# Kernel tuning notes

Hardware: AMD Instinct MI355X
Metric: run time of the kernel (lower is better)

Reference implementation:

```python
import jax, jax.numpy as jnp
import numpy as np

HEADS = 16
D_MODEL = 1024
D_HEAD = D_MODEL // HEADS


def setup_inputs() -> dict:
    key = jax.random.key(0)
    ks = jax.random.split(key, 9)
    s_h = 1.0 / np.sqrt(D_HEAD)
    s_m = 1.0 / np.sqrt(D_MODEL)
    return {
        "x": jax.random.normal(ks[0], (4, 2048, D_MODEL), dtype=jnp.float32),
        "Wq": jax.random.uniform(ks[1], (D_HEAD, D_HEAD), jnp.float32, -s_h, s_h),
        "bq": jax.random.uniform(ks[2], (D_HEAD,), jnp.float32, -s_h, s_h),
        "Wk": jax.random.uniform(ks[3], (D_HEAD, D_HEAD), jnp.float32, -s_h, s_h),
        "bk": jax.random.uniform(ks[4], (D_HEAD,), jnp.float32, -s_h, s_h),
        "Wv": jax.random.uniform(ks[5], (D_HEAD, D_HEAD), jnp.float32, -s_h, s_h),
        "bv": jax.random.uniform(ks[6], (D_HEAD,), jnp.float32, -s_h, s_h),
        "Wp": jax.random.uniform(ks[7], (D_MODEL, D_MODEL), jnp.float32, -s_m, s_m),
        "bp": jax.random.uniform(ks[8], (D_MODEL,), jnp.float32, -s_m, s_m),
    }


def reference(x, Wq, bq, Wk, bk, Wv, bv, Wp, bp):
    B, T, C = x.shape
    xh = x.reshape(B, T, HEADS, D_HEAD)  # [B,T,H,Dh]
    # per-head linear projections (torch Linear: x @ W.T + b)
    q = jnp.einsum('bthd,ed->bhte', xh, Wq) + bq  # [B,H,T,Dh]
    k = jnp.einsum('bthd,ed->bhte', xh, Wk) + bk
    v = jnp.einsum('bthd,ed->bhte', xh, Wv) + bv
    # NOTE: original scales by sqrt(C) = sqrt(d_model), not sqrt(d_head)
    att = jnp.einsum('bhqd,bhkd->bhqk', q, k) / jnp.sqrt(jnp.float32(C))
    att = jax.nn.softmax(att, axis=-1)
    out = jnp.einsum('bhqk,bhkd->bhqd', att, v)  # [B,H,T,Dh]
    out = out.transpose(0, 2, 1, 3).reshape(B, T, C)
    return out @ Wp.T + bp
```

## Files before the change

### kernel.cpp

```cpp
#include <hip/hip_runtime.h>
#include <hip/hip_bf16.h>
#include <cstddef>

#define B_  4
#define T_  2048
#define H_  16
#define DH  64
#define C_  1024
#define BH  64

typedef float  f32x16 __attribute__((ext_vector_type(16)));
typedef __bf16 bf16x8 __attribute__((ext_vector_type(8)));
typedef __bf16 bf16x4 __attribute__((ext_vector_type(4)));

#define MFMA32(a, b, c) __builtin_amdgcn_mfma_f32_32x32x16_bf16(a, b, c, 0, 0, 0)


__device__ __forceinline__ unsigned cvt_pk_bf16(float lo, float hi) {
    unsigned r;
    asm("v_cvt_pk_bf16_f32 %0, %1, %2" : "=v"(r) : "v"(lo), "v"(hi));
    return r;
}

__global__ __launch_bounds__(256) void wconv_kernel(
    const float* __restrict__ Wq, const float* __restrict__ Wk,
    const float* __restrict__ Wv, __bf16* __restrict__ wqkv)
{
    const int tid = blockIdx.x * 256 + threadIdx.x;
    const float* srcs[3] = {Wq, Wk, Wv};
    const int mat = tid >> 10;
    const int off = (tid & 1023) * 4;
    const float4 w4 = *(const float4*)(srcs[mat] + off);
    const unsigned lo = ((unsigned)__builtin_bit_cast(unsigned short, (__bf16)w4.y) << 16)
                      | (unsigned)__builtin_bit_cast(unsigned short, (__bf16)w4.x);
    const unsigned hi = ((unsigned)__builtin_bit_cast(unsigned short, (__bf16)w4.w) << 16)
                      | (unsigned)__builtin_bit_cast(unsigned short, (__bf16)w4.z);
    uint2 p; p.x = lo; p.y = hi;
    *(uint2*)(wqkv + mat * 4096 + off) = p;
}

__global__ __launch_bounds__(256) void qkv_kernel(
    const float* __restrict__ x,
    const __bf16* __restrict__ wqkv,
    const float* __restrict__ bq, const float* __restrict__ bk,
    const float* __restrict__ bv,
    __bf16* __restrict__ q, __bf16* __restrict__ kf, __bf16* __restrict__ vf)
{
    __shared__ __bf16 Xs[128 * 72];
    __shared__ __bf16 Ws[3][64 * 72];
    __bf16* Vtl = Xs;
    __bf16* Kst = &Ws[0][0];

    const int tt  = blockIdx.x;
    const int bh  = blockIdx.y;
    const int b   = bh >> 4, h = bh & 15;
    const int t0  = tt * 128;
    const int tid = threadIdx.x;
    const int wave = tid >> 6, lane = tid & 63;
    const int m = lane & 31, hh = lane >> 5;

    #pragma unroll
    for (int i = 0; i < 8; ++i) {
        const int idx = i * 256 + tid;
        const int r = idx >> 4, c = (idx & 15) * 4;
        const float4 x4 = *(const float4*)(x + ((size_t)(b * T_ + t0 + r)) * C_ + h * DH + c);
        const unsigned lo = ((unsigned)__builtin_bit_cast(unsigned short, (__bf16)x4.y) << 16)
                          | (unsigned)__builtin_bit_cast(unsigned short, (__bf16)x4.x);
        const unsigned hi = ((unsigned)__builtin_bit_cast(unsigned short, (__bf16)x4.w) << 16)
                          | (unsigned)__builtin_bit_cast(unsigned short, (__bf16)x4.z);
        *(unsigned*)&Xs[r * 72 + c]     = lo;
        *(unsigned*)&Xs[r * 72 + c + 2] = hi;
    }
    #pragma unroll
    for (int i = 0; i < 6; ++i) {
        const int idx = i * 256 + tid;
        const int mat_ = idx >> 9;
        const int r = (idx >> 3) & 63, c = (idx & 7) * 8;
        *(uint4*)&Ws[mat_][r * 72 + c] = *(const uint4*)(wqkv + mat_ * 4096 + r * 64 + c);
    }
    __syncthreads();

    bf16x8 xf[4];
    #pragma unroll
    for (int ks = 0; ks < 4; ++ks)
        xf[ks] = *(const bf16x8*)&Xs[(wave * 32 + m) * 72 + ks * 16 + hh * 8];
    __syncthreads();

    const float s32 = 0.03125f * 1.4426950408889634f;

    unsigned kpk[16];

    #pragma unroll
    for (int mat = 0; mat < 3; ++mat) {
        f32x16 acc0 = {}, acc1 = {};
        #pragma unroll
        for (int ks = 0; ks < 4; ++ks) {
            const bf16x8 w0 = *(const bf16x8*)&Ws[mat][(m) * 72 + ks * 16 + hh * 8];
            const bf16x8 w1 = *(const bf16x8*)&Ws[mat][(32 + m) * 72 + ks * 16 + hh * 8];
            acc0 = MFMA32(xf[ks], w0, acc0);
            acc1 = MFMA32(xf[ks], w1, acc1);
        }
        const float* bias = (mat == 0) ? bq : (mat == 1) ? bk : bv;
        const float b0 = bias[m], b1 = bias[32 + m];
        #pragma unroll
        for (int r = 0; r < 16; ++r) {
            const int R = (r & 3) + 8 * (r >> 2) + 4 * hh;
            const int tloc = wave * 32 + R;
            const float v0 = acc0[r] + b0, v1 = acc1[r] + b1;
            if (mat == 0) {
                const size_t base = ((size_t)bh * T_ + t0 + tloc) * DH;
                q[base + m]      = (__bf16)(v0 * s32);
                q[base + 32 + m] = (__bf16)(v1 * s32);
            } else if (mat == 1) {
                kpk[r] = ((unsigned)__builtin_bit_cast(unsigned short, (__bf16)v1) << 16)
                       |  (unsigned)__builtin_bit_cast(unsigned short, (__bf16)v0);
            } else {
                Vtl[(m) * 136 + tloc]      = (__bf16)v0;
                Vtl[(32 + m) * 136 + tloc] = (__bf16)v1;
            }
        }
    }
    __syncthreads();

    #pragma unroll
    for (int r = 0; r < 16; ++r) {
        const int R = (r & 3) + 8 * (r >> 2) + 4 * hh;
        const int tloc = wave * 32 + R;
        Kst[tloc * 72 + m]      = __builtin_bit_cast(__bf16, (unsigned short)(kpk[r] & 0xffff));
        Kst[tloc * 72 + 32 + m] = __builtin_bit_cast(__bf16, (unsigned short)(kpk[r] >> 16));
    }

    #pragma unroll
    for (int i = 0; i < 4; ++i) {
        const int idx = i * 256 + tid;
        const int ln = idx & 63, c_ = idx >> 6;
        const int kt64l = c_ >> 3, dh = (c_ >> 2) & 1, cN = c_ & 3;
        const __bf16* src = &Vtl[(dh * 32 + (ln & 31)) * 136 + kt64l * 64 + cN * 16 + (ln >> 5) * 8];
        __bf16* dst = vf + ((((size_t)(bh * 32 + tt * 2 + kt64l) * 2 + dh) * 4 + cN) * 64 + ln) * 8;
        *(uint4*)dst = *(const uint4*)src;
    }
    __syncthreads();

    #pragma unroll
    for (int i = 0; i < 4; ++i) {
        const int idx = i * 256 + tid;
        const int ln = idx & 63, c_ = idx >> 6;
        const int kt64l = c_ >> 3, rh = (c_ >> 2) & 1, ks = c_ & 3;
        const __bf16* src = &Kst[(kt64l * 64 + rh * 32 + (ln & 31)) * 72 + ks * 16 + (ln >> 5) * 8];
        __bf16* dst = kf + ((((size_t)(bh * 32 + tt * 2 + kt64l) * 2 + rh) * 4 + ks) * 64 + ln) * 8;
        *(uint4*)dst = *(const uint4*)src;
    }
}

__global__ __launch_bounds__(256, 4) void attn_kernel(
    const __bf16* __restrict__ q, const __bf16* __restrict__ kf,
    const __bf16* __restrict__ vf, __bf16* __restrict__ af)
{
    __shared__ float OL[2][64 * 36];
    __shared__ float LL[2][64];

    const int bh  = blockIdx.x;
    const int q0  = blockIdx.y * 64;
    const int tid = threadIdx.x;
    const int wave = tid >> 6, lane = tid & 63;
    const int m = lane & 31, h = lane >> 5;
    const int qs  = wave & 1;
    const int kvh = wave >> 1;

    const __bf16* qb  = q  + (size_t)bh * T_ * DH;
    const __bf16* kfb = kf + (size_t)bh * (T_ * DH);
    const __bf16* vfb = vf + (size_t)bh * (T_ * DH);

    bf16x8 qf[4];
    #pragma unroll
    for (int ks = 0; ks < 4; ++ks)
        qf[ks] = *(const bf16x8*)(qb + (size_t)(q0 + qs * 32 + m) * DH + ks * 16 + h * 8);

    f32x16 O0 = {}, O1 = {};
    float lsum = 0.f;

    const int ktEnd = kvh * 16 + 16;
    for (int kt = kvh * 16; kt < ktEnd; ++kt) {
        const __bf16* kt_k = kfb + kt * 4096;
        const __bf16* kt_v = vfb + kt * 4096;
        #pragma unroll
        for (int rh = 0; rh < 2; ++rh) {
            bf16x8 kfr[4];
            #pragma unroll
            for (int ks = 0; ks < 4; ++ks)
                kfr[ks] = *(const bf16x8*)(kt_k + rh * 2048 + ks * 512 + lane * 8);
            f32x16 S = {};
            #pragma unroll
            for (int ks = 0; ks < 4; ++ks)
                S = MFMA32(kfr[ks], qf[ks], S);

            #pragma unroll
            for (int cc = 0; cc < 2; ++cc) {
                const int rb = cc * 8;
                float e0 = __builtin_amdgcn_exp2f(S[rb + 0]);
                float e1 = __builtin_amdgcn_exp2f(S[rb + 1]);
                float e2 = __builtin_amdgcn_exp2f(S[rb + 2]);
                float e3 = __builtin_amdgcn_exp2f(S[rb + 3]);
                float e4 = __builtin_amdgcn_exp2f(S[rb + 4]);
                float e5 = __builtin_amdgcn_exp2f(S[rb + 5]);
                float e6 = __builtin_amdgcn_exp2f(S[rb + 6]);
                float e7 = __builtin_amdgcn_exp2f(S[rb + 7]);
                lsum += ((e0 + e1) + (e2 + e3)) + ((e4 + e5) + (e6 + e7));
                unsigned a0 = cvt_pk_bf16(e0, e1);
                unsigned a1 = cvt_pk_bf16(e2, e3);
                unsigned b0 = cvt_pk_bf16(e4, e5);
                unsigned b1 = cvt_pk_bf16(e6, e7);
                asm("v_permlane32_swap_b32 %0, %1" : "+v"(a0), "+v"(b0));
                asm("v_permlane32_swap_b32 %0, %1" : "+v"(a1), "+v"(b1));
                const uint4 pw = {a0, a1, b0, b1};
                const bf16x8 pb = __builtin_bit_cast(bf16x8, pw);
                const int c = rh * 2 + cc;
                const bf16x8 v0 = *(const bf16x8*)(kt_v + c * 512 + lane * 8);
                const bf16x8 v1 = *(const bf16x8*)(kt_v + 2048 + c * 512 + lane * 8);
                O0 = MFMA32(v0, pb, O0);
                O1 = MFMA32(v1, pb, O1);
            }
        }
    }

    if (kvh == 1) {
        #pragma unroll
        for (int g = 0; g < 4; ++g) {
            float4 p0, p1;
            p0.x = O0[4 * g];     p0.y = O0[4 * g + 1];
            p0.z = O0[4 * g + 2]; p0.w = O0[4 * g + 3];
            p1.x = O1[4 * g];     p1.y = O1[4 * g + 1];
            p1.z = O1[4 * g + 2]; p1.w = O1[4 * g + 3];
            *(float4*)&OL[qs][lane * 36 + 4 * g]      = p0;
            *(float4*)&OL[qs][lane * 36 + 16 + 4 * g] = p1;
        }
        LL[qs][lane] = lsum;
    }
    __syncthreads();
    if (kvh == 0) {
        #pragma unroll
        for (int g = 0; g < 4; ++g) {
            const float4 p0 = *(const float4*)&OL[qs][lane * 36 + 4 * g];
            const float4 p1 = *(const float4*)&OL[qs][lane * 36 + 16 + 4 * g];
            O0[4 * g]     += p0.x; O0[4 * g + 1] += p0.y;
            O0[4 * g + 2] += p0.z; O0[4 * g + 3] += p0.w;
            O1[4 * g]     += p1.x; O1[4 * g + 1] += p1.y;
            O1[4 * g + 2] += p1.z; O1[4 * g + 3] += p1.w;
        }
        lsum += LL[qs][lane];
        lsum += __shfl_xor(lsum, 32);
        const float linv = 1.0f / lsum;

        __bf16* ab = af + ((size_t)(bh * 16 + (q0 >> 7))) * 8192
                        + (((q0 >> 6) & 1) * 2 + qs) * 2048 + lane * 8;
        #pragma unroll
        for (int ks = 0; ks < 4; ++ks) {
            const f32x16& Og = (ks < 2) ? O0 : O1;
            const int rb = (ks & 1) * 8;
            unsigned a0 = cvt_pk_bf16(Og[rb + 0] * linv, Og[rb + 1] * linv);
            unsigned a1 = cvt_pk_bf16(Og[rb + 2] * linv, Og[rb + 3] * linv);
            unsigned b0 = cvt_pk_bf16(Og[rb + 4] * linv, Og[rb + 5] * linv);
            unsigned b1 = cvt_pk_bf16(Og[rb + 6] * linv, Og[rb + 7] * linv);
            asm("v_permlane32_swap_b32 %0, %1" : "+v"(a0), "+v"(b0));
            asm("v_permlane32_swap_b32 %0, %1" : "+v"(a1), "+v"(b1));
            const uint4 pw = {a0, a1, b0, b1};
            *(uint4*)(ab + ks * 512) = pw;
        }
    }
}

__global__ __launch_bounds__(256) void wpconv_kernel(
    const float* __restrict__ Wp, __bf16* __restrict__ wpf)
{
    const int ci = blockIdx.x * 256 + threadIdx.x;
    const int ln = ci & 63;
    const int ks = (ci >> 6) & 3;
    const int n  = (ci >> 8) & 3;
    const int cb = (ci >> 10) & 15;
    const int eb = ci >> 14;
    const int row = eb * 128 + n * 32 + (ln & 31);
    const int col = cb * 64 + ks * 16 + (ln >> 5) * 8;
    const float4 w0 = *(const float4*)(Wp + (size_t)row * C_ + col);
    const float4 w1 = *(const float4*)(Wp + (size_t)row * C_ + col + 4);
    uint4 p;
    p.x = ((unsigned)__builtin_bit_cast(unsigned short, (__bf16)w0.y) << 16)
        |  (unsigned)__builtin_bit_cast(unsigned short, (__bf16)w0.x);
    p.y = ((unsigned)__builtin_bit_cast(unsigned short, (__bf16)w0.w) << 16)
        |  (unsigned)__builtin_bit_cast(unsigned short, (__bf16)w0.z);
    p.z = ((unsigned)__builtin_bit_cast(unsigned short, (__bf16)w1.y) << 16)
        |  (unsigned)__builtin_bit_cast(unsigned short, (__bf16)w1.x);
    p.w = ((unsigned)__builtin_bit_cast(unsigned short, (__bf16)w1.w) << 16)
        |  (unsigned)__builtin_bit_cast(unsigned short, (__bf16)w1.z);
    *(uint4*)(wpf + (size_t)ci * 8) = p;
}

__global__ __launch_bounds__(256) void proj_kernel(
    const __bf16* __restrict__ af,
    const __bf16* __restrict__ wpf,
    const float* __restrict__ bp,
    float* __restrict__ out)
{
    const int tb2 = blockIdx.x, eb = blockIdx.y;
    const int tid = threadIdx.x;
    const int wave = tid >> 6, lane = tid & 63;
    const int m = lane & 31, h = lane >> 5;
    const int b = tb2 >> 5, rem = tb2 & 31;
    const int qtile = rem >> 1, half = rem & 1;
    const int wv = half * 2 + (wave & 1);
    const int eh = wave >> 1;
    const int e0 = eb * 128;

    const __bf16* abase = af + ((size_t)(b * 256 + qtile)) * 8192
                             + wv * 2048 + lane * 8;
    const __bf16* wbase = wpf + (size_t)eb * 131072 + eh * 4096 + lane * 8;

    f32x16 acc[2] = {f32x16{}, f32x16{}};

    for (int cb = 0; cb < 16; ++cb) {
        const __bf16* ap = abase + (size_t)cb * 131072;
        const __bf16* wp = wbase + (size_t)cb * 8192;
        bf16x8 afr[4];
        #pragma unroll
        for (int ks = 0; ks < 4; ++ks)
            afr[ks] = *(const bf16x8*)(ap + ks * 512);
        #pragma unroll
        for (int n = 0; n < 2; ++n) {
            #pragma unroll
            for (int ks = 0; ks < 4; ++ks) {
                const bf16x8 bf = *(const bf16x8*)(wp + (n * 4 + ks) * 512);
                acc[n] = MFMA32(afr[ks], bf, acc[n]);
            }
        }
    }

    const int tokbase = b * T_ + qtile * 128 + wv * 32;
    #pragma unroll
    for (int n = 0; n < 2; ++n) {
        const int e = e0 + (eh * 2 + n) * 32 + m;
        const float bias = bp[e];
        #pragma unroll
        for (int r = 0; r < 16; ++r) {
            const int R = (r & 3) + 8 * (r >> 2) + 4 * h;
            out[(size_t)(tokbase + R) * C_ + e] = acc[n][r] + bias;
        }
    }
}

extern "C" void kernel_launch(void* const* d_in, const int* in_sizes, int n_in,
                              void* d_out, int out_size, void* d_ws, size_t ws_size,
                              hipStream_t stream)
{
    const float* x  = (const float*)d_in[0];
    const float* Wq = (const float*)d_in[1];
    const float* bq = (const float*)d_in[2];
    const float* Wk = (const float*)d_in[3];
    const float* bk = (const float*)d_in[4];
    const float* Wv = (const float*)d_in[5];
    const float* bv = (const float*)d_in[6];
    const float* Wp = (const float*)d_in[7];
    const float* bp = (const float*)d_in[8];

    const size_t N = (size_t)BH * T_ * DH;
    __bf16* qws  = (__bf16*)d_ws;
    __bf16* kws  = qws + N;
    __bf16* vtws = kws + N;
    __bf16* aws  = vtws + N;
    __bf16* wqkv = aws;
    __bf16* wpf  = qws;

    wconv_kernel<<<dim3(12), 256, 0, stream>>>(Wq, Wk, Wv, wqkv);
    qkv_kernel<<<dim3(16, 64), 256, 0, stream>>>(
        x, wqkv, bq, bk, bv, qws, kws, vtws);
    attn_kernel<<<dim3(64, 32), 256, 0, stream>>>(qws, kws, vtws, aws);
    wpconv_kernel<<<dim3(512), 256, 0, stream>>>(Wp, wpf);
    proj_kernel<<<dim3(128, 8), 256, 0, stream>>>(aws, wpf, bp, (float*)d_out);
}
```

Measured before the change: 230.1 us.

## Give each attention wave 64 query rows over full KV; stage Wp conversion via LDS

After: 230.8 us. About the same (+0.3%).

```diff
diff --git a/kernel.cpp b/kernel.cpp
--- a/kernel.cpp
+++ b/kernel.cpp
@@ -152,35 +152,32 @@
     }
 }
 
-__global__ __launch_bounds__(256, 4) void attn_kernel(
+__global__ __launch_bounds__(256, 2) void attn_kernel(
     const __bf16* __restrict__ q, const __bf16* __restrict__ kf,
     const __bf16* __restrict__ vf, __bf16* __restrict__ af)
 {
-    __shared__ float OL[2][64 * 36];
-    __shared__ float LL[2][64];
-
     const int bh  = blockIdx.x;
-    const int q0  = blockIdx.y * 64;
+    const int q0  = blockIdx.y * 256;
     const int tid = threadIdx.x;
     const int wave = tid >> 6, lane = tid & 63;
     const int m = lane & 31, h = lane >> 5;
-    const int qs  = wave & 1;
-    const int kvh = wave >> 1;
+    const int row0 = q0 + wave * 64;
 
     const __bf16* qb  = q  + (size_t)bh * T_ * DH;
     const __bf16* kfb = kf + (size_t)bh * (T_ * DH);
     const __bf16* vfb = vf + (size_t)bh * (T_ * DH);
 
-    bf16x8 qf[4];
-    #pragma unroll
-    for (int ks = 0; ks < 4; ++ks)
-        qf[ks] = *(const bf16x8*)(qb + (size_t)(q0 + qs * 32 + m) * DH + ks * 16 + h * 8);
-
-    f32x16 O0 = {}, O1 = {};
-    float lsum = 0.f;
-
-    const int ktEnd = kvh * 16 + 16;
-    for (int kt = kvh * 16; kt < ktEnd; ++kt) {
+    bf16x8 qfa[4], qfb_[4];
+    #pragma unroll
+    for (int ks = 0; ks < 4; ++ks) {
+        qfa[ks]  = *(const bf16x8*)(qb + (size_t)(row0 + m) * DH + ks * 16 + h * 8);
+        qfb_[ks] = *(const bf16x8*)(qb + (size_t)(row0 + 32 + m) * DH + ks * 16 + h * 8);
+    }
+
+    f32x16 Oa0 = {}, Oa1 = {}, Ob0 = {}, Ob1 = {};
+    float lsa = 0.f, lsb = 0.f;
+
+    for (int kt = 0; kt < 32; ++kt) {
         const __bf16* kt_k = kfb + kt * 4096;
         const __bf16* kt_v = vfb + kt * 4096;
         #pragma unroll
@@ -189,82 +186,95 @@
             #pragma unroll
             for (int ks = 0; ks < 4; ++ks)
                 kfr[ks] = *(const bf16x8*)(kt_k + rh * 2048 + ks * 512 + lane * 8);
-            f32x16 S = {};
+            f32x16 Sa = {}, Sb = {};
             #pragma unroll
-            for (int ks = 0; ks < 4; ++ks)
-                S = MFMA32(kfr[ks], qf[ks], S);
+            for (int ks = 0; ks < 4; ++ks) {
+                Sa = MFMA32(kfr[ks], qfa[ks],  Sa);
+                Sb = MFMA32(kfr[ks], qfb_[ks], Sb);
+            }
 
             #pragma unroll
             for (int cc = 0; cc < 2; ++cc) {
                 const int rb = cc * 8;
-                float e0 = __builtin_amdgcn_exp2f(S[rb + 0]);
-                float e1 = __builtin_amdgcn_exp2f(S[rb + 1]);
-                float e2 = __builtin_amdgcn_exp2f(S[rb + 2]);
-                float e3 = __builtin_amdgcn_exp2f(S[rb + 3]);
-                float e4 = __builtin_amdgcn_exp2f(S[rb + 4]);
-                float e5 = __builtin_amdgcn_exp2f(S[rb + 5]);
-                float e6 = __builtin_amdgcn_exp2f(S[rb + 6]);
-                float e7 = __builtin_amdgcn_exp2f(S[rb + 7]);
-                lsum += ((e0 + e1) + (e2 + e3)) + ((e4 + e5) + (e6 + e7));
-                unsigned a0 = cvt_pk_bf16(e0, e1);
-                unsigned a1 = cvt_pk_bf16(e2, e3);
-                unsigned b0 = cvt_pk_bf16(e4, e5);
-                unsigned b1 = cvt_pk_bf16(e6, e7);
-                asm("v_permlane32_swap_b32 %0, %1" : "+v"(a0), "+v"(b0));
-                asm("v_permlane32_swap_b32 %0, %1" : "+v"(a1), "+v"(b1));
-                const uint4 pw = {a0, a1, b0, b1};
-                const bf16x8 pb = __builtin_bit_cast(bf16x8, pw);
+                float a0f = __builtin_amdgcn_exp2f(Sa[rb + 0]);
+                float a1f = __builtin_amdgcn_exp2f(Sa[rb + 1]);
+                float a2f = __builtin_amdgcn_exp2f(Sa[rb + 2]);
+                float a3f = __builtin_amdgcn_exp2f(Sa[rb + 3]);
+                float a4f = __builtin_amdgcn_exp2f(Sa[rb + 4]);
+                float a5f = __builtin_amdgcn_exp2f(Sa[rb + 5]);
+                float a6f = __builtin_amdgcn_exp2f(Sa[rb + 6]);
+                float a7f = __builtin_amdgcn_exp2f(Sa[rb + 7]);
+                lsa += ((a0f + a1f) + (a2f + a3f)) + ((a4f + a5f) + (a6f + a7f));
+                unsigned pa0 = cvt_pk_bf16(a0f, a1f);
+                unsigned pa1 = cvt_pk_bf16(a2f, a3f);
+                unsigned pa2 = cvt_pk_bf16(a4f, a5f);
+                unsigned pa3 = cvt_pk_bf16(a6f, a7f);
+                asm("v_permlane32_swap_b32 %0, %1" : "+v"(pa0), "+v"(pa2));
+                asm("v_permlane32_swap_b32 %0, %1" : "+v"(pa1), "+v"(pa3));
+                const uint4 pwa = {pa0, pa1, pa2, pa3};
+                const bf16x8 pba = __builtin_bit_cast(bf16x8, pwa);
+                float b0f = __builtin_amdgcn_exp2f(Sb[rb + 0]);
+                float b1f = __builtin_amdgcn_exp2f(Sb[rb + 1]);
+                float b2f = __builtin_amdgcn_exp2f(Sb[rb + 2]);
+                float b3f = __builtin_amdgcn_exp2f(Sb[rb + 3]);
+                float b4f = __builtin_amdgcn_exp2f(Sb[rb + 4]);
+                float b5f = __builtin_amdgcn_exp2f(Sb[rb + 5]);
+                float b6f = __builtin_amdgcn_exp2f(Sb[rb + 6]);
+                float b7f = __builtin_amdgcn_exp2f(Sb[rb + 7]);
+                lsb += ((b0f + b1f) + (b2f + b3f)) + ((b4f + b5f) + (b6f + b7f));
+                unsigned pb0 = cvt_pk_bf16(b0f, b1f);
+                unsigned pb1 = cvt_pk_bf16(b2f, b3f);
+                unsigned pb2 = cvt_pk_bf16(b4f, b5f);
+                unsigned pb3 = cvt_pk_bf16(b6f, b7f);
+                asm("v_permlane32_swap_b32 %0, %1" : "+v"(pb0), "+v"(pb2));
+                asm("v_permlane32_swap_b32 %0, %1" : "+v"(pb1), "+v"(pb3));
+                const uint4 pwb = {pb0, pb1, pb2, pb3};
+                const bf16x8 pbb = __builtin_bit_cast(bf16x8, pwb);
+
                 const int c = rh * 2 + cc;
                 const bf16x8 v0 = *(const bf16x8*)(kt_v + c * 512 + lane * 8);
                 const bf16x8 v1 = *(const bf16x8*)(kt_v + 2048 + c * 512 + lane * 8);
-                O0 = MFMA32(v0, pb, O0);
-                O1 = MFMA32(v1, pb, O1);
+                Oa0 = MFMA32(v0, pba, Oa0);
+                Oa1 = MFMA32(v1, pba, Oa1);
+                Ob0 = MFMA32(v0, pbb, Ob0);
+                Ob1 = MFMA32(v1, pbb, Ob1);
             }
         }
     }
 
-    if (kvh == 1) {
-        #pragma unroll
-        for (int g = 0; g < 4; ++g) {
-            float4 p0, p1;
-            p0.x = O0[4 * g];     p0.y = O0[4 * g + 1];
-            p0.z = O0[4 * g + 2]; p0.w = O0[4 * g + 3];
-            p1.x = O1[4 * g];     p1.y = O1[4 * g + 1];
-            p1.z = O1[4 * g + 2]; p1.w = O1[4 * g + 3];
-            *(float4*)&OL[qs][lane * 36 + 4 * g]      = p0;
-            *(float4*)&OL[qs][lane * 36 + 16 + 4 * g] = p1;
-        }
-        LL[qs][lane] = lsum;
-    }
-    __syncthreads();
-    if (kvh == 0) {
-        #pragma unroll
-        for (int g = 0; g < 4; ++g) {
-            const float4 p0 = *(const float4*)&OL[qs][lane * 36 + 4 * g];
-            const float4 p1 = *(const float4*)&OL[qs][lane * 36 + 16 + 4 * g];
-            O0[4 * g]     += p0.x; O0[4 * g + 1] += p0.y;
-            O0[4 * g + 2] += p0.z; O0[4 * g + 3] += p0.w;
-            O1[4 * g]     += p1.x; O1[4 * g + 1] += p1.y;
-            O1[4 * g + 2] += p1.z; O1[4 * g + 3] += p1.w;
-        }
-        lsum += LL[qs][lane];
-        lsum += __shfl_xor(lsum, 32);
-        const float linv = 1.0f / lsum;
-
-        __bf16* ab = af + ((size_t)(bh * 16 + (q0 >> 7))) * 8192
-                        + (((q0 >> 6) & 1) * 2 + qs) * 2048 + lane * 8;
-        #pragma unroll
-        for (int ks = 0; ks < 4; ++ks) {
-            const f32x16& Og = (ks < 2) ? O0 : O1;
+    lsa += __shfl_xor(lsa, 32);
+    lsb += __shfl_xor(lsb, 32);
+    const float linva = 1.0f / lsa, linvb = 1.0f / lsb;
+
+    const int qt = row0 >> 7;
+    const int wv_a = (row0 >> 5) & 3;
+    __bf16* ab_a = af + ((size_t)(bh * 16 + qt)) * 8192 + wv_a * 2048 + lane * 8;
+    __bf16* ab_b = ab_a + 2048;
+    #pragma unroll
+    for (int ks = 0; ks < 4; ++ks) {
+        {
+            const f32x16& Og = (ks < 2) ? Oa0 : Oa1;
             const int rb = (ks & 1) * 8;
-            unsigned a0 = cvt_pk_bf16(Og[rb + 0] * linv, Og[rb + 1] * linv);
-            unsigned a1 = cvt_pk_bf16(Og[rb + 2] * linv, Og[rb + 3] * linv);
-            unsigned b0 = cvt_pk_bf16(Og[rb + 4] * linv, Og[rb + 5] * linv);
-            unsigned b1 = cvt_pk_bf16(Og[rb + 6] * linv, Og[rb + 7] * linv);
+            unsigned a0 = cvt_pk_bf16(Og[rb + 0] * linva, Og[rb + 1] * linva);
+            unsigned a1 = cvt_pk_bf16(Og[rb + 2] * linva, Og[rb + 3] * linva);
+            unsigned b0 = cvt_pk_bf16(Og[rb + 4] * linva, Og[rb + 5] * linva);
+            unsigned b1 = cvt_pk_bf16(Og[rb + 6] * linva, Og[rb + 7] * linva);
             asm("v_permlane32_swap_b32 %0, %1" : "+v"(a0), "+v"(b0));
             asm("v_permlane32_swap_b32 %0, %1" : "+v"(a1), "+v"(b1));
             const uint4 pw = {a0, a1, b0, b1};
-            *(uint4*)(ab + ks * 512) = pw;
+            *(uint4*)(ab_a + ks * 512) = pw;
+        }
+        {
+            const f32x16& Og = (ks < 2) ? Ob0 : Ob1;
+            const int rb = (ks & 1) * 8;
+            unsigned a0 = cvt_pk_bf16(Og[rb + 0] * linvb, Og[rb + 1] * linvb);
+            unsigned a1 = cvt_pk_bf16(Og[rb + 2] * linvb, Og[rb + 3] * linvb);
+            unsigned b0 = cvt_pk_bf16(Og[rb + 4] * linvb, Og[rb + 5] * linvb);
+            unsigned b1 = cvt_pk_bf16(Og[rb + 6] * linvb, Og[rb + 7] * linvb);
+            asm("v_permlane32_swap_b32 %0, %1" : "+v"(a0), "+v"(b0));
+            asm("v_permlane32_swap_b32 %0, %1" : "+v"(a1), "+v"(b1));
+            const uint4 pw = {a0, a1, b0, b1};
+            *(uint4*)(ab_b + ks * 512) = pw;
         }
     }
 }
@@ -272,26 +282,35 @@
 __global__ __launch_bounds__(256) void wpconv_kernel(
     const float* __restrict__ Wp, __bf16* __restrict__ wpf)
 {
-    const int ci = blockIdx.x * 256 + threadIdx.x;
-    const int ln = ci & 63;
-    const int ks = (ci >> 6) & 3;
-    const int n  = (ci >> 8) & 3;
-    const int cb = (ci >> 10) & 15;
-    const int eb = ci >> 14;
-    const int row = eb * 128 + n * 32 + (ln & 31);
-    const int col = cb * 64 + ks * 16 + (ln >> 5) * 8;
-    const float4 w0 = *(const float4*)(Wp + (size_t)row * C_ + col);
-    const float4 w1 = *(const float4*)(Wp + (size_t)row * C_ + col + 4);
-    uint4 p;
-    p.x = ((unsigned)__builtin_bit_cast(unsigned short, (__bf16)w0.y) << 16)
-        |  (unsigned)__builtin_bit_cast(unsigned short, (__bf16)w0.x);
-    p.y = ((unsigned)__builtin_bit_cast(unsigned short, (__bf16)w0.w) << 16)
-        |  (unsigned)__builtin_bit_cast(unsigned short, (__bf16)w0.z);
-    p.z = ((unsigned)__builtin_bit_cast(unsigned short, (__bf16)w1.y) << 16)
-        |  (unsigned)__builtin_bit_cast(unsigned short, (__bf16)w1.x);
-    p.w = ((unsigned)__builtin_bit_cast(unsigned short, (__bf16)w1.w) << 16)
-        |  (unsigned)__builtin_bit_cast(unsigned short, (__bf16)w1.z);
-    *(uint4*)(wpf + (size_t)ci * 8) = p;
+    __shared__ __bf16 Bs[128 * 72];
+
+    const int t  = blockIdx.x;
+    const int eb = t >> 4, cb = t & 15;
+    const int tid = threadIdx.x;
+
+    #pragma unroll
+    for (int i = 0; i < 8; ++i) {
+        const int idx = i * 256 + tid;
+        const int r = idx >> 4, c = (idx & 15) * 4;
+        const float4 w4 = *(const float4*)(Wp + (size_t)(eb * 128 + r) * C_ + cb * 64 + c);
+        const unsigned lo = ((unsigned)__builtin_bit_cast(unsigned short, (__bf16)w4.y) << 16)
+                          | (unsigned)__builtin_bit_cast(unsigned short, (__bf16)w4.x);
+        const unsigned hi = ((unsigned)__builtin_bit_cast(unsigned short, (__bf16)w4.w) << 16)
+                          | (unsigned)__builtin_bit_cast(unsigned short, (__bf16)w4.z);
+        *(unsigned*)&Bs[r * 72 + c]     = lo;
+        *(unsigned*)&Bs[r * 72 + c + 2] = hi;
+    }
+    __syncthreads();
+
+    #pragma unroll
+    for (int i = 0; i < 4; ++i) {
+        const int idx = i * 256 + tid;
+        const int ln = idx & 63, c_ = idx >> 6;
+        const int n = c_ >> 2, ks = c_ & 3;
+        const __bf16* src = &Bs[(n * 32 + (ln & 31)) * 72 + ks * 16 + (ln >> 5) * 8];
+        *(uint4*)(wpf + (size_t)eb * 131072 + cb * 8192 + c_ * 512 + ln * 8)
+            = *(const uint4*)src;
+    }
 }
 
 __global__ __launch_bounds__(256) void proj_kernel(
@@ -371,7 +390,7 @@
     wconv_kernel<<<dim3(12), 256, 0, stream>>>(Wq, Wk, Wv, wqkv);
     qkv_kernel<<<dim3(16, 64), 256, 0, stream>>>(
         x, wqkv, bq, bk, bv, qws, kws, vtws);
-    attn_kernel<<<dim3(64, 32), 256, 0, stream>>>(qws, kws, vtws, aws);
-    wpconv_kernel<<<dim3(512), 256, 0, stream>>>(Wp, wpf);
+    attn_kernel<<<dim3(64, 8), 256, 0, stream>>>(qws, kws, vtws, aws);
+    wpconv_kernel<<<dim3(128), 256, 0, stream>>>(Wp, wpf);
     proj_kernel<<<dim3(128, 8), 256, 0, stream>>>(aws, wpf, bp, (float*)d_out);
 }
```
